# Performance work log

Hardware: AMD Instinct MI355X
Metric: run time of the kernel (lower is better)

## Reference

```python
import jax, jax.numpy as jnp
import numpy as np

EMB = 1024
HEADS = 16
HEAD_DIM = EMB // HEADS
CTX = 2048
BATCH = 4
LN_EPS = 1e-5


def layer_norm(x, g, b):
    mu = jnp.mean(x, axis=-1, keepdims=True)
    var = jnp.mean(jnp.square(x - mu), axis=-1, keepdims=True)
    return (x - mu) * jax.lax.rsqrt(var + LN_EPS) * g + b


def setup_inputs() -> dict:
    key = jax.random.key(0)
    ks = jax.random.split(key, 12)
    s_in = 1.0 / np.sqrt(EMB)
    s_ff = 1.0 / np.sqrt(4 * EMB)
    return {
        "x": jax.random.normal(ks[0], (BATCH, CTX, EMB), jnp.float32),
        # per-head Q/K/V projections, no bias (matches Head linears)
        "wq": jax.random.normal(ks[1], (HEADS, EMB, HEAD_DIM), jnp.float32) * s_in,
        "wk": jax.random.normal(ks[2], (HEADS, EMB, HEAD_DIM), jnp.float32) * s_in,
        "wv": jax.random.normal(ks[3], (HEADS, EMB, HEAD_DIM), jnp.float32) * s_in,
        "w_proj": jax.random.normal(ks[4], (EMB, EMB), jnp.float32) * s_in,
        "b_proj": jnp.zeros((EMB,), jnp.float32),
        "w1": jax.random.normal(ks[5], (EMB, 4 * EMB), jnp.float32) * s_in,
        "b1": jnp.zeros((4 * EMB,), jnp.float32),
        "w2": jax.random.normal(ks[6], (4 * EMB, EMB), jnp.float32) * s_ff,
        "b2": jnp.zeros((EMB,), jnp.float32),
        "ln1_g": jnp.ones((EMB,), jnp.float32),
        "ln1_b": jnp.zeros((EMB,), jnp.float32),
        "ln2_g": jnp.ones((EMB,), jnp.float32),
        "ln2_b": jnp.zeros((EMB,), jnp.float32),
    }


def reference(x, wq, wk, wv, w_proj, b_proj, w1, b1, w2, b2, ln1_g, ln1_b, ln2_g, ln2_b):
    B, T, C = x.shape
    # --- attention branch (pre-LN) ---
    h = layer_norm(x, ln1_g, ln1_b)
    q = jnp.einsum('btc,hcd->bhtd', h, wq)
    k = jnp.einsum('btc,hcd->bhtd', h, wk)
    v = jnp.einsum('btc,hcd->bhtd', h, wv)
    scale = 1.0 / np.sqrt(HEAD_DIM)
    scores = jnp.einsum('bhtd,bhsd->bhts', q, k) * scale  # [B,H,T,T]
    causal = jnp.tril(jnp.ones((T, T), dtype=bool))
    scores = jnp.where(causal, scores, -jnp.inf)
    attn = jax.nn.softmax(scores, axis=-1)
    out = jnp.einsum('bhts,bhsd->bhtd', attn, v)
    out = out.transpose(0, 2, 1, 3).reshape(B, T, C)  # concat heads
    out = out @ w_proj.T + b_proj if False else jnp.einsum('btc,cd->btd', out, w_proj) + b_proj
    x = x + out
    # --- FFN branch (pre-LN) ---
    h2 = layer_norm(x, ln2_g, ln2_b)
    ff = jax.nn.relu(jnp.einsum('btc,cf->btf', h2, w1) + b1)
    ff = jnp.einsum('btf,fc->btc', ff, w2) + b2
    return x + ff
```

## Files before the change

kernel.cpp:

```cpp
#include <hip/hip_runtime.h>


#define DEVI __device__ __forceinline__

typedef float  f32x4  __attribute__((ext_vector_type(4)));
typedef float  f32x16 __attribute__((ext_vector_type(16)));
typedef __bf16 bf16x8 __attribute__((ext_vector_type(8)));
typedef short  s16x8  __attribute__((ext_vector_type(8)));
typedef unsigned int u32x4 __attribute__((ext_vector_type(4)));
typedef unsigned short u16;

DEVI u16 f2bf(float f) {
    return __builtin_bit_cast(u16, (__bf16)f);
}

DEVI unsigned pk2(float lo, float hi2) {
    return (unsigned)f2bf(lo) | ((unsigned)f2bf(hi2) << 16);
}

DEVI void gload_lds16(const void* g, void* l) {
    __builtin_amdgcn_global_load_lds(
        (__attribute__((address_space(1))) void*)(g),
        (__attribute__((address_space(3))) void*)(l), 16, 0, 0);
}

DEVI f32x4 mfma16(s16x8 a, s16x8 b, f32x4 c) {
    return __builtin_amdgcn_mfma_f32_16x16x32_bf16(
        __builtin_bit_cast(bf16x8, a), __builtin_bit_cast(bf16x8, b), c, 0, 0, 0);
}

DEVI f32x16 mfma32(s16x8 a, s16x8 b, f32x16 c) {
    return __builtin_amdgcn_mfma_f32_32x32x16_bf16(
        __builtin_bit_cast(bf16x8, a), __builtin_bit_cast(bf16x8, b), c, 0, 0, 0);
}

__global__ __launch_bounds__(256) void transpose_cvt(
    const float* __restrict__ src, u16* __restrict__ dst,
    int K, int N, long srcStride, long dstStride)
{
    __shared__ float t[64][65];
    src += (long)blockIdx.z * srcStride;
    dst += (long)blockIdx.z * dstStride;
    int k0 = blockIdx.x * 64, n0 = blockIdx.y * 64;
    int tx = threadIdx.x & 63, ty = threadIdx.x >> 6;
#pragma unroll
    for (int i = 0; i < 16; ++i) {
        int r = ty * 16 + i;
        t[r][tx] = src[(long)(k0 + r) * N + n0 + tx];
    }
    __syncthreads();
#pragma unroll
    for (int i = 0; i < 16; ++i) {
        int r = ty * 16 + i;
        dst[(long)(n0 + r) * K + k0 + tx] = f2bf(t[tx][r]);
    }
}

__global__ __launch_bounds__(256) void ln_bf16(
    const float* __restrict__ x, const float* __restrict__ g,
    const float* __restrict__ b, u16* __restrict__ out)
{
    int row = blockIdx.x, tid = threadIdx.x;
    const float4 v = ((const float4*)(x + (long)row * 1024))[tid];
    float s = v.x + v.y + v.z + v.w;
    float q = v.x * v.x + v.y * v.y + v.z * v.z + v.w * v.w;
#pragma unroll
    for (int m = 1; m < 64; m <<= 1) { s += __shfl_xor(s, m); q += __shfl_xor(q, m); }
    __shared__ float red[8];
    int lane = tid & 63, w = tid >> 6;
    if (lane == 0) { red[w] = s; red[w + 4] = q; }
    __syncthreads();
    s = red[0] + red[1] + red[2] + red[3];
    q = red[4] + red[5] + red[6] + red[7];
    float mu  = s * (1.0f / 1024.0f);
    float var = q * (1.0f / 1024.0f) - mu * mu;
    float rs  = rsqrtf(var + 1e-5f);
    float4 gv = ((const float4*)g)[tid];
    float4 bv = ((const float4*)b)[tid];
    ushort4 o;
    o.x = f2bf((v.x - mu) * rs * gv.x + bv.x);
    o.y = f2bf((v.y - mu) * rs * gv.y + bv.y);
    o.z = f2bf((v.z - mu) * rs * gv.z + bv.z);
    o.w = f2bf((v.w - mu) * rs * gv.w + bv.w);
    ((ushort4*)(out + (long)row * 1024))[tid] = o;
}

template <int EPI>
__global__ __launch_bounds__(256, 3) void gemm_bt(
    const u16* __restrict__ A, const u16* __restrict__ Bt,
    int M, int N, int K,
    float* __restrict__ outF, u16* __restrict__ outB,
    const float* __restrict__ bias, const float* __restrict__ resid,
    u16* __restrict__ qd, u16* __restrict__ kd, u16* __restrict__ vd)
{
    __shared__ alignas(16) u16 As[128 * 32];
    __shared__ alignas(16) u16 Bs[128 * 32];
    int tid = threadIdx.x;
    int lane = tid & 63, w = tid >> 6;
    int wm = w & 1, wn = w >> 1;
    int l15 = lane & 15, l4 = lane >> 4;
    long m0 = (long)blockIdx.x * 128, n0 = (long)blockIdx.y * 128;
    const u16* Ag = A + m0 * K;
    const u16* Bg = Bt + n0 * K;
    int scol = (lane & 3) * 8;
    int srow0 = (w * 2 + 0) * 16 + (lane >> 2);
    int srow1 = (w * 2 + 1) * 16 + (lane >> 2);

    f32x4 acc[4][4] = {};

    for (int kt = 0; kt < K; kt += 32) {
        gload_lds16(Ag + (long)srow0 * K + kt + scol, &As[(w * 2 + 0) * 512]);
        gload_lds16(Ag + (long)srow1 * K + kt + scol, &As[(w * 2 + 1) * 512]);
        gload_lds16(Bg + (long)srow0 * K + kt + scol, &Bs[(w * 2 + 0) * 512]);
        gload_lds16(Bg + (long)srow1 * K + kt + scol, &Bs[(w * 2 + 1) * 512]);
        __syncthreads();
        s16x8 a[4], b[4];
#pragma unroll
        for (int m = 0; m < 4; ++m)
            a[m] = *(const s16x8*)&As[(wm * 64 + m * 16 + l15) * 32 + l4 * 8];
#pragma unroll
        for (int n = 0; n < 4; ++n)
            b[n] = *(const s16x8*)&Bs[(wn * 64 + n * 16 + l15) * 32 + l4 * 8];
#pragma unroll
        for (int m = 0; m < 4; ++m)
#pragma unroll
            for (int n = 0; n < 4; ++n)
                acc[m][n] = mfma16(a[m], b[n], acc[m][n]);
        __syncthreads();
    }

    long mbase = m0 + wm * 64;
    long nbase = n0 + wn * 64;
#pragma unroll
    for (int m = 0; m < 4; ++m)
#pragma unroll
        for (int n = 0; n < 4; ++n)
#pragma unroll
            for (int r = 0; r < 4; ++r) {
                long row = mbase + m * 16 + l4 * 4 + r;
                long col = nbase + n * 16 + l15;
                float val = acc[m][n][r];
                if constexpr (EPI == 0) {
                    int c = (int)col;
                    int which = c >> 10, hh = (c >> 6) & 15, dd = c & 63;
                    int bb = (int)(row >> 11), tt = (int)(row & 2047);
                    if (which == 2) {
                        vd[((long)(bb * 16 + hh) * 64 + dd) * 2048 + tt] = f2bf(val);
                    } else {
                        u16* dst = which == 0 ? qd : kd;
                        dst[((long)(bb * 16 + hh) * 2048 + tt) * 64 + dd] = f2bf(val);
                    }
                } else if constexpr (EPI == 1) {
                    outF[row * N + col] = val + bias[col] + resid[row * N + col];
                } else {
                    float t2 = val + bias[col];
                    outB[row * N + col] = f2bf(t2 > 0.f ? t2 : 0.f);
                }
            }
}

__global__ __launch_bounds__(256, 4) void attn_kernel(
    const u16* __restrict__ Q, const u16* __restrict__ K,
    const u16* __restrict__ Vt, u16* __restrict__ O)
{
    constexpr int PAD = 72;
    constexpr float SC2 = 0.125f * 1.44269504088896f;
    constexpr float THR = 11.5416f;
    __shared__ alignas(16) u16 Ks[2][64 * PAD];
    __shared__ alignas(16) u16 Vts[2][64 * PAD];
    __shared__ alignas(16) float xbuf[4][32];
    int tid = threadIdx.x, lane = tid & 63, w = tid >> 6;
    int l31 = lane & 31, hi = lane >> 5;
    bool h = (hi != 0);
    int qp = blockIdx.x, hh = blockIdx.y, bb = blockIdx.z;
    const long hbase = ((long)(bb * 16 + hh)) * 2048 * 64;

    int srow[2], scol8[2];
#pragma unroll
    for (int i = 0; i < 2; ++i) {
        int c = tid + 256 * i;
        srow[i] = c >> 3;
        scol8[i] = (c & 7) * 8;
    }

#pragma unroll 1
    for (int ph = 0; ph < 2; ++ph) {
        int qt = ph == 0 ? qp : 15 - qp;
        int q0w = qt * 128 + w * 32;
        int nt = 2 * qt + 2;
        int qv = q0w + l31;

        s16x8 bq[4];
#pragma unroll
        for (int c = 0; c < 4; ++c)
            bq[c] = *(const s16x8*)&Q[hbase + (long)(q0w + l31) * 64 + c * 16 + hi * 8];

        f32x16 o0 = {}, o1 = {};
        float mrow = -1e30f, lrow = 0.f;

        s16x8 kr[2], vr[2];
        {
            const u16* Kg = K + hbase;
            const u16* Vg = Vt + hbase;
#pragma unroll
            for (int i = 0; i < 2; ++i) {
                s16x8 k0 = *(const s16x8*)&Kg[srow[i] * 64 + scol8[i]];
                s16x8 v0 = *(const s16x8*)&Vg[(long)srow[i] * 2048 + scol8[i]];
                *(s16x8*)&Ks[0][srow[i] * PAD + scol8[i]]  = k0;
                *(s16x8*)&Vts[0][srow[i] * PAD + scol8[i]] = v0;
            }
            if (nt > 1) {
                const u16* Kg1 = K + hbase + 64 * 64;
                const u16* Vg1 = Vt + hbase + 64;
#pragma unroll
                for (int i = 0; i < 2; ++i) {
                    kr[i] = *(const s16x8*)&Kg1[srow[i] * 64 + scol8[i]];
                    vr[i] = *(const s16x8*)&Vg1[(long)srow[i] * 2048 + scol8[i]];
                }
            }
        }
        __syncthreads();

#pragma unroll 1
        for (int kt = 0; kt < nt; ++kt) {
            int cur = kt & 1;
            if (kt + 1 < nt) {
#pragma unroll
                for (int i = 0; i < 2; ++i) {
                    *(s16x8*)&Ks[cur ^ 1][srow[i] * PAD + scol8[i]]  = kr[i];
                    *(s16x8*)&Vts[cur ^ 1][srow[i] * PAD + scol8[i]] = vr[i];
                }
            }
            if (kt + 2 < nt) {
                const u16* Kg = K + hbase + (long)(kt + 2) * 64 * 64;
                const u16* Vg = Vt + hbase + (long)(kt + 2) * 64;
#pragma unroll
                for (int i = 0; i < 2; ++i) {
                    kr[i] = *(const s16x8*)&Kg[srow[i] * 64 + scol8[i]];
                    vr[i] = *(const s16x8*)&Vg[(long)srow[i] * 2048 + scol8[i]];
                }
            }

#pragma unroll
            for (int k2 = 0; k2 < 2; ++k2) {
                int kbase = kt * 64 + k2 * 32;
                if (kbase <= q0w + 31) {
                    f32x16 s = {};
                    __builtin_amdgcn_s_setprio(1);
#pragma unroll
                    for (int c = 0; c < 4; ++c) {
                        s16x8 ak = *(const s16x8*)&Ks[cur][(k2 * 32 + l31) * PAD + c * 16 + hi * 8];
                        s = mfma32(ak, bq[c], s);
                    }
                    __builtin_amdgcn_s_setprio(0);

                    int khi = kbase + 4 * hi;
                    if (kbase + 31 > q0w) {
#pragma unroll
                        for (int r = 0; r < 16; ++r) {
                            int kg = khi + ((r & 3) + 8 * (r >> 2));
                            float sv = s[r] * SC2;
                            s[r] = (kg > qv) ? -1e30f : sv;
                        }
                    } else {
#pragma unroll
                        for (int r = 0; r < 16; ++r) s[r] *= SC2;
                    }

                    float t8[8], t4[4], t2[2];
#pragma unroll
                    for (int r = 0; r < 8; ++r) t8[r] = fmaxf(s[r], s[r + 8]);
#pragma unroll
                    for (int r = 0; r < 4; ++r) t4[r] = fmaxf(t8[r], t8[r + 4]);
                    t2[0] = fmaxf(t4[0], t4[2]); t2[1] = fmaxf(t4[1], t4[3]);
                    float pm = fmaxf(t2[0], t2[1]);
                    pm = fmaxf(pm, __shfl_xor(pm, 32));

                    int allok = __all(pm - mrow <= THR);
                    float ef = 1.f;
                    if (!allok) {
                        float mn = fmaxf(mrow, pm);
                        ef = exp2f(mrow - mn);
                        mrow = mn;
                    }
                    float a8[8], a4[4];
#pragma unroll
                    for (int r = 0; r < 16; ++r) s[r] = exp2f(s[r] - mrow);
#pragma unroll
                    for (int r = 0; r < 8; ++r) a8[r] = s[r] + s[r + 8];
#pragma unroll
                    for (int r = 0; r < 4; ++r) a4[r] = a8[r] + a8[r + 4];
                    float rsum = (a4[0] + a4[1]) + (a4[2] + a4[3]);
                    rsum += __shfl_xor(rsum, 32);

                    if (!allok) {
                        lrow = lrow * ef + rsum;
                        xbuf[w][l31] = ef;
#pragma unroll
                        for (int rr = 0; rr < 4; ++rr) {
                            f32x4 efv = *(const f32x4*)&xbuf[w][rr * 8 + hi * 4];
#pragma unroll
                            for (int j = 0; j < 4; ++j) {
                                o0[rr * 4 + j] *= efv[j];
                                o1[rr * 4 + j] *= efv[j];
                            }
                        }
                    } else {
                        lrow += rsum;
                    }

                    unsigned c0 = pk2(s[0],  s[1]),  c1 = pk2(s[2],  s[3]);
                    unsigned c2 = pk2(s[4],  s[5]),  c3 = pk2(s[6],  s[7]);
                    unsigned c4 = pk2(s[8],  s[9]),  c5 = pk2(s[10], s[11]);
                    unsigned c6 = pk2(s[12], s[13]), c7 = pk2(s[14], s[15]);
                    unsigned x0 = __shfl_xor((int)c0, 32), x1 = __shfl_xor((int)c1, 32);
                    unsigned x2 = __shfl_xor((int)c2, 32), x3 = __shfl_xor((int)c3, 32);
                    unsigned x4 = __shfl_xor((int)c4, 32), x5 = __shfl_xor((int)c5, 32);
                    unsigned x6 = __shfl_xor((int)c6, 32), x7 = __shfl_xor((int)c7, 32);
                    u32x4 w0 = { h ? x2 : c0, h ? x3 : c1, h ? c2 : x0, h ? c3 : x1 };
                    u32x4 w1 = { h ? x6 : c4, h ? x7 : c5, h ? c6 : x4, h ? c7 : x5 };
                    s16x8 pa0 = __builtin_bit_cast(s16x8, w0);
                    s16x8 pa1 = __builtin_bit_cast(s16x8, w1);

                    __builtin_amdgcn_s_setprio(1);
#pragma unroll
                    for (int ks = 0; ks < 2; ++ks) {
                        s16x8 pa = ks ? pa1 : pa0;
                        s16x8 bv0 = *(const s16x8*)&Vts[cur][(l31) * PAD + k2 * 32 + ks * 16 + hi * 8];
                        s16x8 bv1 = *(const s16x8*)&Vts[cur][(32 + l31) * PAD + k2 * 32 + ks * 16 + hi * 8];
                        o0 = mfma32(pa, bv0, o0);
                        o1 = mfma32(pa, bv1, o1);
                    }
                    __builtin_amdgcn_s_setprio(0);
                }
            }
            __syncthreads();
        }

        float il = 1.0f / lrow;
        xbuf[w][l31] = il;
        f32x4 ilv[4];
#pragma unroll
        for (int rr = 0; rr < 4; ++rr)
            ilv[rr] = *(const f32x4*)&xbuf[w][rr * 8 + hi * 4];
#pragma unroll
        for (int r = 0; r < 16; ++r) {
            int t = q0w + ((r & 3) + 8 * (r >> 2)) + 4 * hi;
            float sc = ilv[r >> 2][r & 3];
            long rbase = ((long)(bb * 2048 + t)) * 1024 + hh * 64;
            O[rbase + l31]      = f2bf(o0[r] * sc);
            O[rbase + 32 + l31] = f2bf(o1[r] * sc);
        }
        __syncthreads();
    }
}

extern "C" void kernel_launch(void* const* d_in, const int* in_sizes, int n_in,
                              void* d_out, int out_size, void* d_ws, size_t ws_size,
                              hipStream_t stream)
{
    const float* x      = (const float*)d_in[0];
    const float* wq     = (const float*)d_in[1];
    const float* wk     = (const float*)d_in[2];
    const float* wv     = (const float*)d_in[3];
    const float* w_proj = (const float*)d_in[4];
    const float* b_proj = (const float*)d_in[5];
    const float* w1     = (const float*)d_in[6];
    const float* b1     = (const float*)d_in[7];
    const float* w2     = (const float*)d_in[8];
    const float* b2     = (const float*)d_in[9];
    const float* ln1_g  = (const float*)d_in[10];
    const float* ln1_b  = (const float*)d_in[11];
    const float* ln2_g  = (const float*)d_in[12];
    const float* ln2_b  = (const float*)d_in[13];

    char* ws = (char*)d_ws;
    u16*   WQKVt = (u16*)(ws + 0);
    u16*   WPt   = (u16*)(ws + 6291456);
    u16*   W1t   = (u16*)(ws + 8388608);
    u16*   W2t   = (u16*)(ws + 16777216);
    u16*   H     = (u16*)(ws + 25165824);
    u16*   Qb    = (u16*)(ws + 41943040);
    u16*   Kb    = (u16*)(ws + 58720256);
    u16*   Vb    = (u16*)(ws + 75497472);
    u16*   Ob    = (u16*)(ws + 92274688);
    u16*   FF    = (u16*)(ws + 41943040);
    float* X1    = (float*)(ws + 109051904);
    float* out   = (float*)d_out;

    transpose_cvt<<<dim3(16, 1, 16), 256, 0, stream>>>(wq, WQKVt,           1024, 64, 65536, 65536);
    transpose_cvt<<<dim3(16, 1, 16), 256, 0, stream>>>(wk, WQKVt + 1048576, 1024, 64, 65536, 65536);
    transpose_cvt<<<dim3(16, 1, 16), 256, 0, stream>>>(wv, WQKVt + 2097152, 1024, 64, 65536, 65536);
    transpose_cvt<<<dim3(16, 16, 1), 256, 0, stream>>>(w_proj, WPt, 1024, 1024, 0, 0);
    transpose_cvt<<<dim3(16, 64, 1), 256, 0, stream>>>(w1, W1t, 1024, 4096, 0, 0);
    transpose_cvt<<<dim3(64, 16, 1), 256, 0, stream>>>(w2, W2t, 4096, 1024, 0, 0);

    ln_bf16<<<8192, 256, 0, stream>>>(x, ln1_g, ln1_b, H);

    gemm_bt<0><<<dim3(64, 24), 256, 0, stream>>>(H, WQKVt, 8192, 3072, 1024,
        nullptr, nullptr, nullptr, nullptr, Qb, Kb, Vb);

    attn_kernel<<<dim3(8, 16, 4), 256, 0, stream>>>(Qb, Kb, Vb, Ob);

    gemm_bt<1><<<dim3(64, 8), 256, 0, stream>>>(Ob, WPt, 8192, 1024, 1024,
        X1, nullptr, b_proj, x, nullptr, nullptr, nullptr);

    ln_bf16<<<8192, 256, 0, stream>>>(X1, ln2_g, ln2_b, H);

    gemm_bt<2><<<dim3(64, 32), 256, 0, stream>>>(H, W1t, 8192, 4096, 1024,
        nullptr, FF, b1, nullptr, nullptr, nullptr, nullptr);

    gemm_bt<1><<<dim3(64, 8), 256, 0, stream>>>(FF, W2t, 8192, 1024, 4096,
        out, nullptr, b2, X1, nullptr, nullptr, nullptr);
}
```

Measured before the change: 427.7 us.

## Split causal attention key range across two blocks and merge with combine kernel

Each query tile's key range is now split into two halves computed by different blocks. This doubles the attention grid while keeping per-block work balanced through the p / 15-p pairing, and aims to raise occupancy on the many CUs. Each block writes unnormalized bf16 partial outputs plus the row max and row sum. A new combine kernel rescales and merges the two partials into the head-concatenated layout. The cost is an extra launch, extra global traffic for the partials, and bf16 rounding of unnormalized partials.

```diff
diff --git a/kernel.cpp b/kernel.cpp
--- a/kernel.cpp
+++ b/kernel.cpp
@@ -12,6 +12,11 @@
 
 DEVI u16 f2bf(float f) {
     return __builtin_bit_cast(u16, (__bf16)f);
+}
+
+DEVI float bf2f(u16 u) {
+    unsigned v = (unsigned)u << 16;
+    return __builtin_bit_cast(float, v);
 }
 
 DEVI unsigned pk2(float lo, float hi2) {
@@ -159,9 +164,10 @@
             }
 }
 
-__global__ __launch_bounds__(256, 4) void attn_kernel(
+__global__ __launch_bounds__(256, 4) void attn_split(
     const u16* __restrict__ Q, const u16* __restrict__ K,
-    const u16* __restrict__ Vt, u16* __restrict__ O)
+    const u16* __restrict__ Vt,
+    u16* __restrict__ Op0, u16* __restrict__ Op1, float* __restrict__ ML)
 {
     constexpr int PAD = 72;
     constexpr float SC2 = 0.125f * 1.44269504088896f;
@@ -172,8 +178,9 @@
     int tid = threadIdx.x, lane = tid & 63, w = tid >> 6;
     int l31 = lane & 31, hi = lane >> 5;
     bool h = (hi != 0);
-    int qp = blockIdx.x, hh = blockIdx.y, bb = blockIdx.z;
+    int p = blockIdx.x, hh = blockIdx.y, bb = blockIdx.z;
     const long hbase = ((long)(bb * 16 + hh)) * 2048 * 64;
+    const long rb = ((long)(bb * 16 + hh)) * 2048;
 
     int srow[2], scol8[2];
 #pragma unroll
@@ -185,9 +192,11 @@
 
 #pragma unroll 1
     for (int ph = 0; ph < 2; ++ph) {
-        int qt = ph == 0 ? qp : 15 - qp;
+        int qt  = ph == 0 ? p : 15 - p;
+        int kt0 = ph == 0 ? 0 : (qt + 1);
+        int kt1 = qt + 1 + ph * (qt + 1);
+        int ntl = kt1 - kt0;
         int q0w = qt * 128 + w * 32;
-        int nt = 2 * qt + 2;
         int qv = q0w + l31;
 
         s16x8 bq[4];
@@ -200,8 +209,8 @@
 
         s16x8 kr[2], vr[2];
         {
-            const u16* Kg = K + hbase;
-            const u16* Vg = Vt + hbase;
+            const u16* Kg = K + hbase + (long)kt0 * 64 * 64;
+            const u16* Vg = Vt + hbase + (long)kt0 * 64;
 #pragma unroll
             for (int i = 0; i < 2; ++i) {
                 s16x8 k0 = *(const s16x8*)&Kg[srow[i] * 64 + scol8[i]];
@@ -209,9 +218,9 @@
                 *(s16x8*)&Ks[0][srow[i] * PAD + scol8[i]]  = k0;
                 *(s16x8*)&Vts[0][srow[i] * PAD + scol8[i]] = v0;
             }
-            if (nt > 1) {
-                const u16* Kg1 = K + hbase + 64 * 64;
-                const u16* Vg1 = Vt + hbase + 64;
+            if (ntl > 1) {
+                const u16* Kg1 = K + hbase + (long)(kt0 + 1) * 64 * 64;
+                const u16* Vg1 = Vt + hbase + (long)(kt0 + 1) * 64;
 #pragma unroll
                 for (int i = 0; i < 2; ++i) {
                     kr[i] = *(const s16x8*)&Kg1[srow[i] * 64 + scol8[i]];
@@ -222,16 +231,17 @@
         __syncthreads();
 
 #pragma unroll 1
-        for (int kt = 0; kt < nt; ++kt) {
-            int cur = kt & 1;
-            if (kt + 1 < nt) {
+        for (int j = 0; j < ntl; ++j) {
+            int kt = kt0 + j;
+            int cur = j & 1;
+            if (j + 1 < ntl) {
 #pragma unroll
                 for (int i = 0; i < 2; ++i) {
                     *(s16x8*)&Ks[cur ^ 1][srow[i] * PAD + scol8[i]]  = kr[i];
                     *(s16x8*)&Vts[cur ^ 1][srow[i] * PAD + scol8[i]] = vr[i];
                 }
             }
-            if (kt + 2 < nt) {
+            if (j + 2 < ntl) {
                 const u16* Kg = K + hbase + (long)(kt + 2) * 64 * 64;
                 const u16* Vg = Vt + hbase + (long)(kt + 2) * 64;
 #pragma unroll
@@ -300,9 +310,9 @@
                         for (int rr = 0; rr < 4; ++rr) {
                             f32x4 efv = *(const f32x4*)&xbuf[w][rr * 8 + hi * 4];
 #pragma unroll
-                            for (int j = 0; j < 4; ++j) {
-                                o0[rr * 4 + j] *= efv[j];
-                                o1[rr * 4 + j] *= efv[j];
+                            for (int j2 = 0; j2 < 4; ++j2) {
+                                o0[rr * 4 + j2] *= efv[j2];
+                                o1[rr * 4 + j2] *= efv[j2];
                             }
                         }
                     } else {
@@ -337,22 +347,44 @@
             __syncthreads();
         }
 
-        float il = 1.0f / lrow;
-        xbuf[w][l31] = il;
-        f32x4 ilv[4];
-#pragma unroll
-        for (int rr = 0; rr < 4; ++rr)
-            ilv[rr] = *(const f32x4*)&xbuf[w][rr * 8 + hi * 4];
+        u16* Ops = ph ? Op1 : Op0;
 #pragma unroll
         for (int r = 0; r < 16; ++r) {
             int t = q0w + ((r & 3) + 8 * (r >> 2)) + 4 * hi;
-            float sc = ilv[r >> 2][r & 3];
-            long rbase = ((long)(bb * 2048 + t)) * 1024 + hh * 64;
-            O[rbase + l31]      = f2bf(o0[r] * sc);
-            O[rbase + 32 + l31] = f2bf(o1[r] * sc);
+            long ro = (rb + t) * 64;
+            Ops[ro + l31]      = f2bf(o0[r]);
+            Ops[ro + 32 + l31] = f2bf(o1[r]);
+        }
+        if (hi == 0) {
+            long mrow_i = rb + q0w + l31;
+            ML[ph * 262144 + mrow_i]          = mrow;
+            ML[ph * 262144 + 131072 + mrow_i] = lrow;
         }
         __syncthreads();
     }
+}
+
+__global__ __launch_bounds__(256) void attn_combine(
+    const u16* __restrict__ Op0, const u16* __restrict__ Op1,
+    const float* __restrict__ ML, u16* __restrict__ O)
+{
+    int tid = threadIdx.x;
+    long row = (long)blockIdx.x * 16 + (tid >> 4);
+    int d0 = (tid & 15) * 4;
+    float m1 = ML[row],          l1 = ML[131072 + row];
+    float m2 = ML[262144 + row], l2 = ML[393216 + row];
+    float mm = fmaxf(m1, m2);
+    float w1 = exp2f(m1 - mm), w2 = exp2f(m2 - mm);
+    float inv = 1.0f / (w1 * l1 + w2 * l2);
+    ushort4 a = *(const ushort4*)&Op0[row * 64 + d0];
+    ushort4 b = *(const ushort4*)&Op1[row * 64 + d0];
+    ushort4 o;
+    o.x = f2bf((w1 * bf2f(a.x) + w2 * bf2f(b.x)) * inv);
+    o.y = f2bf((w1 * bf2f(a.y) + w2 * bf2f(b.y)) * inv);
+    o.z = f2bf((w1 * bf2f(a.z) + w2 * bf2f(b.z)) * inv);
+    o.w = f2bf((w1 * bf2f(a.w) + w2 * bf2f(b.w)) * inv);
+    int bb = (int)(row >> 15), hh2 = (int)((row >> 11) & 15), t = (int)(row & 2047);
+    *(ushort4*)&O[((long)(bb * 2048 + t)) * 1024 + hh2 * 64 + d0] = o;
 }
 
 extern "C" void kernel_launch(void* const* d_in, const int* in_sizes, int n_in,
@@ -380,13 +412,17 @@
     u16*   W1t   = (u16*)(ws + 8388608);
     u16*   W2t   = (u16*)(ws + 16777216);
     u16*   H     = (u16*)(ws + 25165824);
+    float* ML    = (float*)(ws + 25165824 + 8388608);
     u16*   Qb    = (u16*)(ws + 41943040);
     u16*   Kb    = (u16*)(ws + 58720256);
     u16*   Vb    = (u16*)(ws + 75497472);
     u16*   Ob    = (u16*)(ws + 92274688);
     u16*   FF    = (u16*)(ws + 41943040);
     float* X1    = (float*)(ws + 109051904);
+    u16*   Op0   = (u16*)(ws + 109051904);
+    u16*   Op1   = (u16*)(ws + 109051904 + 16777216);
     float* out   = (float*)d_out;
+    ML = (float*)(ws + 25165824);
 
     transpose_cvt<<<dim3(16, 1, 16), 256, 0, stream>>>(wq, WQKVt,           1024, 64, 65536, 65536);
     transpose_cvt<<<dim3(16, 1, 16), 256, 0, stream>>>(wk, WQKVt + 1048576, 1024, 64, 65536, 65536);
@@ -400,7 +436,8 @@
     gemm_bt<0><<<dim3(64, 24), 256, 0, stream>>>(H, WQKVt, 8192, 3072, 1024,
         nullptr, nullptr, nullptr, nullptr, Qb, Kb, Vb);
 
-    attn_kernel<<<dim3(8, 16, 4), 256, 0, stream>>>(Qb, Kb, Vb, Ob);
+    attn_split<<<dim3(16, 16, 4), 256, 0, stream>>>(Qb, Kb, Vb, Op0, Op1, ML);
+    attn_combine<<<8192, 256, 0, stream>>>(Op0, Op1, ML, Ob);
 
     gemm_bt<1><<<dim3(64, 8), 256, 0, stream>>>(Ob, WPt, 8192, 1024, 1024,
         X1, nullptr, b_proj, x, nullptr, nullptr, nullptr);
```

Result: no change. 425.6 us (-0.5%).
